# Kernel optimization log

Hardware: AMD Instinct MI355X
Metric: run time of the kernel (lower is better)

Reference implementation:

```python
import jax, jax.numpy as jnp
import numpy as np

# Propagation forward (reference path), with:
#   pairwise_fn       = dot product over feature dim: scores[b,i,j] = <val[b,i], val[b,j]>
#   edge_compress_fn  = softsign(x) = x / (1 + |x|)
#   val_proj/state_proj = Identity, return_delta = True
# Output: concat(delta_val [B,N,D], delta_state [B,N,1]) -> [B,N,D+1]

B, N, D = 4, 4096, 256


def setup_inputs() -> dict:
    key = jax.random.key(0)
    k1, k2 = jax.random.split(key)
    val = jax.random.normal(k1, (B, N, D), dtype=jnp.float32)
    state = jax.random.normal(k2, (B, N), dtype=jnp.float32)
    return {"val": val, "state": state}


def reference(val, state):
    # pairwise scores over all node pairs: [B, N, N]
    scores = jnp.einsum("bid,bjd->bij", val, val)
    # softsign edge compression
    edges = scores / (1.0 + jnp.abs(scores))
    # delta_state[b,i] = sum_j edges[b,i,j] * state[b,j]
    delta_state = jnp.einsum("bij,bj->bi", edges, state)
    # delta_val[b,i,d] = sum_j edges[b,i,j] * val[b,j,d]
    delta_val = jnp.einsum("bij,bjd->bid", edges, val)
    return jnp.concatenate([delta_val, delta_state[..., None]], axis=-1)
```

## Files before the change

kernel.cpp:

```cpp
#include <hip/hip_runtime.h>
#include <stdint.h>

#define BATCH 4
#define NN 4096
#define DD 256
#define TI 128
#define TJ 64
#define JS 2
#define JRANGE (NN / JS)
#define NITER (JRANGE / TJ)

#define VS_OFF 0
#define VT_OFF 65536
#define P_OFF  131072
#define LDS_BYTES 163840

typedef __attribute__((ext_vector_type(8))) short bf16x8;
typedef __attribute__((ext_vector_type(4))) float f32x4;
typedef __attribute__((ext_vector_type(4))) float f4v;
typedef __attribute__((ext_vector_type(8))) short s8v;
typedef __attribute__((ext_vector_type(4))) short s4v;

__device__ __forceinline__ short f2bf(float f) {
    uint32_t u = __builtin_bit_cast(uint32_t, f);
    u = (u + 0x7fffu + ((u >> 16) & 1u)) >> 16;
    return (short)u;
}

__device__ __forceinline__ void g2l16(const void* g, void* l) {
    __builtin_amdgcn_global_load_lds((const __attribute__((address_space(1))) void*)g,
                                     (__attribute__((address_space(3))) void*)l, 16, 0, 0);
}

__global__ __launch_bounds__(256) void prep_k(const float* __restrict__ val,
                                              short* __restrict__ vbf,
                                              short* __restrict__ vt) {
    __shared__ float tile[32][33];
    int b = blockIdx.z;
    int d0 = blockIdx.x * 32, n0 = blockIdx.y * 32;
    int tx = threadIdx.x, ty = threadIdx.y;
#pragma unroll
    for (int yy = ty; yy < 32; yy += 8) {
        float v = val[((size_t)b * NN + n0 + yy) * DD + d0 + tx];
        tile[yy][tx] = v;
        vbf[((size_t)b * NN + n0 + yy) * DD + d0 + tx] = f2bf(v);
    }
    __syncthreads();
#pragma unroll
    for (int yy = ty; yy < 32; yy += 8)
        vt[((size_t)b * DD + d0 + yy) * NN + n0 + tx] = f2bf(tile[tx][yy]);
}

__global__ void __launch_bounds__(512, 2) prop_main(const short* __restrict__ vbf,
                                                    const short* __restrict__ vtbf,
                                                    const float* __restrict__ state,
                                                    float* __restrict__ part,
                                                    float* __restrict__ spart) {
    extern __shared__ char smem[];

    const int raw = blockIdx.x;
    const int bid = ((raw & 7) << 5) | (raw >> 3);
    const int js = (bid >> 5) & 1;
    const int rb = bid & 31;
    const int b = bid >> 6;
    const int tid = threadIdx.x;
    const int w = tid >> 6, lane = tid & 63;
    const int g = lane >> 4, c = lane & 15;
    const int ig = w & 3, jh = w >> 2;
    const int wr = w & 1, wd = w >> 1;
    const int r7 = c & 7;
    const int j0base = js * JRANGE;

    const int xE = ((((r7 >> 2) << 2) | (g ^ (r7 & 3))) << 4);
    const int xO = (((((r7 >> 2) ^ 1) << 2) | (g ^ (r7 & 3))) << 4);

    bf16x8 Bf[2][8];
    const size_t irowb = (size_t)b * NN + rb * TI + ig * 32;
#pragma unroll
    for (int m = 0; m < 2; ++m)
#pragma unroll
        for (int k = 0; k < 8; ++k)
            Bf[m][k] = *(const bf16x8*)(vbf + ((irowb + m * 16 + c) * DD + k * 32 + g * 8));

    f32x4 accO[4][4];
#pragma unroll
    for (int mt = 0; mt < 4; ++mt)
#pragma unroll
        for (int dt = 0; dt < 4; ++dt)
            accO[mt][dt] = (f32x4){0.f, 0.f, 0.f, 0.f};
    float vsum[2] = {0.f, 0.f};

    auto stageVs = [&](int t, int nb) {
        const int j0 = j0base + t * TJ;
        char* dst = smem + VS_OFF + nb * 32768;
#pragma unroll
        for (int p = 0; p < 4; ++p) {
            int ch0 = p * 512 + w * 64;
            int ch = ch0 + lane;
            int row = ch >> 5, cir = ch & 31;
            g2l16(vbf + ((size_t)(b * NN + j0 + row) * DD + ((cir ^ (row & 7)) * 8)),
                  dst + ch0 * 16);
        }
    };
    auto stageVt = [&](int t, int nb) {
        const int j0 = j0base + t * TJ;
        char* dst = smem + VT_OFF + nb * 32768;
#pragma unroll
        for (int p = 0; p < 4; ++p) {
            int ch0 = p * 512 + w * 64;
            int ch = ch0 + lane;
            int d = ch >> 3, cj = ch & 7;
            g2l16(vtbf + ((size_t)(b * DD + d) * NN + j0 + ((cj ^ (d & 7)) * 8)),
                  dst + ch0 * 16);
        }
    };

    auto pvStep = [&](int slot) {
        const char* paRow = smem + P_OFF + slot * 16384 + (wr * 64 + c) * 128;
        const char* vbRow = smem + VT_OFF + slot * 32768 + (wd * 64 + c) * 128;
        __builtin_amdgcn_s_setprio(1);
#pragma unroll
        for (int kk = 0; kk < 2; ++kk) {
            const int off = kk ? xO : xE;
            bf16x8 pa[4], vb[4];
#pragma unroll
            for (int mt = 0; mt < 4; ++mt) pa[mt] = *(const bf16x8*)(paRow + mt * 2048 + off);
#pragma unroll
            for (int dt = 0; dt < 4; ++dt) vb[dt] = *(const bf16x8*)(vbRow + dt * 2048 + off);
#pragma unroll
            for (int mt = 0; mt < 4; ++mt)
#pragma unroll
                for (int dt = 0; dt < 4; ++dt)
                    accO[mt][dt] = __builtin_amdgcn_mfma_f32_16x16x32_bf16(pa[mt], vb[dt], accO[mt][dt], 0, 0, 0);
        }
        __builtin_amdgcn_s_setprio(0);
    };

    const float* stp = state + b * NN + j0base;

    stageVs(0, 0);
    stageVt(0, 0);
    __syncthreads();

    for (int t = 0; t < NITER; ++t) {
        const int cur = t & 1, prv = cur ^ 1;

        if (t + 1 < NITER) stageVs(t + 1, prv);

        f4v sv0 = *(const f4v*)(stp + t * TJ + jh * 32 + g * 4);
        f4v sv1 = *(const f4v*)(stp + t * TJ + jh * 32 + 16 + g * 4);

        if (t > 0) pvStep(prv);

        f32x4 accS[2][2];
#pragma unroll
        for (int jbl = 0; jbl < 2; ++jbl)
#pragma unroll
            for (int m = 0; m < 2; ++m)
                accS[jbl][m] = (f32x4){0.f, 0.f, 0.f, 0.f};

        const char* aRow0 = smem + VS_OFF + cur * 32768 + (jh * 32 + c) * 512;
        __builtin_amdgcn_s_setprio(1);
#pragma unroll
        for (int k = 0; k < 8; ++k) {
            const int off = (k >> 1) * 128 + ((k & 1) ? xO : xE);
            bf16x8 a0 = *(const bf16x8*)(aRow0 + off);
            bf16x8 a1 = *(const bf16x8*)(aRow0 + 8192 + off);
            accS[0][0] = __builtin_amdgcn_mfma_f32_16x16x32_bf16(a0, Bf[0][k], accS[0][0], 0, 0, 0);
            accS[0][1] = __builtin_amdgcn_mfma_f32_16x16x32_bf16(a0, Bf[1][k], accS[0][1], 0, 0, 0);
            accS[1][0] = __builtin_amdgcn_mfma_f32_16x16x32_bf16(a1, Bf[0][k], accS[1][0], 0, 0, 0);
            accS[1][1] = __builtin_amdgcn_mfma_f32_16x16x32_bf16(a1, Bf[1][k], accS[1][1], 0, 0, 0);
        }
        __builtin_amdgcn_s_setprio(0);

#pragma unroll
        for (int jbl = 0; jbl < 2; ++jbl) {
            f4v sv = jbl ? sv1 : sv0;
#pragma unroll
            for (int m = 0; m < 2; ++m) {
                s4v pk;
#pragma unroll
                for (int r = 0; r < 4; ++r) {
                    float s = accS[jbl][m][r];
                    float e = s * __builtin_amdgcn_rcpf(1.0f + __builtin_fabsf(s));
                    vsum[m] += e * sv[r];
                    pk[r] = f2bf(e);
                }
                int i = ig * 32 + m * 16 + c;
                *(s4v*)(smem + P_OFF + cur * 16384 + i * 128 +
                        ((jh * 64 + jbl * 32 + g * 8) ^ (r7 << 4))) = pk;
            }
        }

        __syncthreads();

        if (t + 1 < NITER) stageVt(t + 1, prv);
    }

    pvStep((NITER - 1) & 1);

    {
        float* po = part + (((size_t)(js * BATCH + b) * NN + rb * TI + wr * 64) * DD) + wd * 64;
#pragma unroll
        for (int mt = 0; mt < 4; ++mt)
#pragma unroll
            for (int dt = 0; dt < 4; ++dt)
#pragma unroll
                for (int r = 0; r < 4; ++r)
                    po[(size_t)(mt * 16 + g * 4 + r) * DD + dt * 16 + c] = accO[mt][dt][r];
    }

#pragma unroll
    for (int m = 0; m < 2; ++m) {
        vsum[m] += __shfl_xor(vsum[m], 16);
        vsum[m] += __shfl_xor(vsum[m], 32);
    }
    float* Xf = (float*)(smem + P_OFF);
    __syncthreads();
    if (jh == 1 && lane < 16) {
        Xf[(ig * 2 + 0) * 16 + lane] = vsum[0];
        Xf[(ig * 2 + 1) * 16 + lane] = vsum[1];
    }
    __syncthreads();
    if (jh == 0 && lane < 16) {
        size_t sb = ((size_t)js * BATCH + b) * NN + rb * TI + ig * 32;
#pragma unroll
        for (int m = 0; m < 2; ++m)
            spart[sb + m * 16 + lane] = vsum[m] + Xf[(ig * 2 + m) * 16 + lane];
    }
}

__global__ __launch_bounds__(256) void reduce2_k(const float* __restrict__ part,
                                                 const float* __restrict__ spart,
                                                 float* __restrict__ out) {
    const int row = blockIdx.x;
    const int t = threadIdx.x;
    const size_t PS = (size_t)BATCH * NN * DD;
    float v = part[(size_t)row * DD + t] + part[PS + (size_t)row * DD + t];
    out[(size_t)row * 257 + t] = v;
    if (t == 0) {
        const size_t SS = (size_t)BATCH * NN;
        out[(size_t)row * 257 + 256] = spart[row] + spart[SS + row];
    }
}

extern "C" void kernel_launch(void* const* d_in, const int* in_sizes, int n_in,
                              void* d_out, int out_size, void* d_ws, size_t ws_size,
                              hipStream_t stream) {
    const float* val = (const float*)d_in[0];
    const float* state = (const float*)d_in[1];
    float* out = (float*)d_out;

    const size_t bf_bytes = (size_t)BATCH * NN * DD * 2;
    const size_t part_bytes = (size_t)JS * BATCH * NN * DD * 4;
    const size_t spart_bytes = (size_t)JS * BATCH * NN * 4;
    short* vbf = (short*)d_ws;
    short* vtbf = (short*)((char*)d_ws + bf_bytes);
    float* part = (float*)((char*)d_ws + 2 * bf_bytes);
    float* spart = (float*)((char*)d_ws + 2 * bf_bytes + part_bytes);
    if (ws_size < 2 * bf_bytes + part_bytes + spart_bytes) return;

    hipFuncSetAttribute((const void*)prop_main, hipFuncAttributeMaxDynamicSharedMemorySize, LDS_BYTES);

    prep_k<<<dim3(DD / 32, NN / 32, BATCH), dim3(32, 8), 0, stream>>>(val, vbf, vtbf);
    prop_main<<<BATCH * (NN / TI) * JS, 512, LDS_BYTES, stream>>>(vbf, vtbf, state, part, spart);
    reduce2_k<<<BATCH * NN, 256, 0, stream>>>(part, spart, out);
}
```

Baseline: 94.41 us.

## Double workgroup to 1024 threads and repartition score/PV work across 16 waves

Prop kernel now runs 16 waves per block instead of 8. Each wave computes a 16x32 score tile and a 32x64 output tile, halving per-wave accumulators and staging loads. The score MFMAs are moved ahead of the previous PV step, and setprio is dropped around them. The state partial sums are reduced across four j-quarters through LDS. Launch bounds (1024,4) ask for fewer registers per thread, which may cause spills. LDS usage per block is unchanged, so resident waves per CU go up but blocks per CU may not.

```diff
diff --git a/kernel.cpp b/kernel.cpp
--- a/kernel.cpp
+++ b/kernel.cpp
@@ -31,6 +31,10 @@
     __builtin_amdgcn_global_load_lds((const __attribute__((address_space(1))) void*)g,
                                      (__attribute__((address_space(3))) void*)l, 16, 0, 0);
 }
+__device__ __forceinline__ void g2l4(const void* g, void* l) {
+    __builtin_amdgcn_global_load_lds((const __attribute__((address_space(1))) void*)g,
+                                     (__attribute__((address_space(3))) void*)l, 4, 0, 0);
+}
 
 __global__ __launch_bounds__(256) void prep_k(const float* __restrict__ val,
                                               short* __restrict__ vbf,
@@ -51,11 +55,11 @@
         vt[((size_t)b * DD + d0 + yy) * NN + n0 + tx] = f2bf(tile[tx][yy]);
 }
 
-__global__ void __launch_bounds__(512, 2) prop_main(const short* __restrict__ vbf,
-                                                    const short* __restrict__ vtbf,
-                                                    const float* __restrict__ state,
-                                                    float* __restrict__ part,
-                                                    float* __restrict__ spart) {
+__global__ void __launch_bounds__(1024, 4) prop_main(const short* __restrict__ vbf,
+                                                     const short* __restrict__ vtbf,
+                                                     const float* __restrict__ state,
+                                                     float* __restrict__ part,
+                                                     float* __restrict__ spart) {
     extern __shared__ char smem[];
 
     const int raw = blockIdx.x;
@@ -66,8 +70,8 @@
     const int tid = threadIdx.x;
     const int w = tid >> 6, lane = tid & 63;
     const int g = lane >> 4, c = lane & 15;
-    const int ig = w & 3, jh = w >> 2;
-    const int wr = w & 1, wd = w >> 1;
+    const int jq = w & 3, ip = w >> 2;
+    const int id = w >> 2, dq = w & 3;
     const int r7 = c & 7;
     const int j0base = js * JRANGE;
 
@@ -75,16 +79,16 @@
     const int xO = (((((r7 >> 2) ^ 1) << 2) | (g ^ (r7 & 3))) << 4);
 
     bf16x8 Bf[2][8];
-    const size_t irowb = (size_t)b * NN + rb * TI + ig * 32;
+    const size_t irowb = (size_t)b * NN + rb * TI + ip * 32;
 #pragma unroll
     for (int m = 0; m < 2; ++m)
 #pragma unroll
         for (int k = 0; k < 8; ++k)
             Bf[m][k] = *(const bf16x8*)(vbf + ((irowb + m * 16 + c) * DD + k * 32 + g * 8));
 
-    f32x4 accO[4][4];
-#pragma unroll
-    for (int mt = 0; mt < 4; ++mt)
+    f32x4 accO[2][4];
+#pragma unroll
+    for (int mt = 0; mt < 2; ++mt)
 #pragma unroll
         for (int dt = 0; dt < 4; ++dt)
             accO[mt][dt] = (f32x4){0.f, 0.f, 0.f, 0.f};
@@ -94,8 +98,8 @@
         const int j0 = j0base + t * TJ;
         char* dst = smem + VS_OFF + nb * 32768;
 #pragma unroll
-        for (int p = 0; p < 4; ++p) {
-            int ch0 = p * 512 + w * 64;
+        for (int p = 0; p < 2; ++p) {
+            int ch0 = p * 1024 + w * 64;
             int ch = ch0 + lane;
             int row = ch >> 5, cir = ch & 31;
             g2l16(vbf + ((size_t)(b * NN + j0 + row) * DD + ((cir ^ (row & 7)) * 8)),
@@ -106,8 +110,8 @@
         const int j0 = j0base + t * TJ;
         char* dst = smem + VT_OFF + nb * 32768;
 #pragma unroll
-        for (int p = 0; p < 4; ++p) {
-            int ch0 = p * 512 + w * 64;
+        for (int p = 0; p < 2; ++p) {
+            int ch0 = p * 1024 + w * 64;
             int ch = ch0 + lane;
             int d = ch >> 3, cj = ch & 7;
             g2l16(vtbf + ((size_t)(b * DD + d) * NN + j0 + ((cj ^ (d & 7)) * 8)),
@@ -116,19 +120,19 @@
     };
 
     auto pvStep = [&](int slot) {
-        const char* paRow = smem + P_OFF + slot * 16384 + (wr * 64 + c) * 128;
-        const char* vbRow = smem + VT_OFF + slot * 32768 + (wd * 64 + c) * 128;
+        const char* paRow = smem + P_OFF + slot * 16384 + (id * 32 + c) * 128;
+        const char* vbRow = smem + VT_OFF + slot * 32768 + (dq * 64 + c) * 128;
         __builtin_amdgcn_s_setprio(1);
 #pragma unroll
         for (int kk = 0; kk < 2; ++kk) {
             const int off = kk ? xO : xE;
-            bf16x8 pa[4], vb[4];
-#pragma unroll
-            for (int mt = 0; mt < 4; ++mt) pa[mt] = *(const bf16x8*)(paRow + mt * 2048 + off);
+            bf16x8 pa[2], vb[4];
+#pragma unroll
+            for (int mt = 0; mt < 2; ++mt) pa[mt] = *(const bf16x8*)(paRow + mt * 2048 + off);
 #pragma unroll
             for (int dt = 0; dt < 4; ++dt) vb[dt] = *(const bf16x8*)(vbRow + dt * 2048 + off);
 #pragma unroll
-            for (int mt = 0; mt < 4; ++mt)
+            for (int mt = 0; mt < 2; ++mt)
 #pragma unroll
                 for (int dt = 0; dt < 4; ++dt)
                     accO[mt][dt] = __builtin_amdgcn_mfma_f32_16x16x32_bf16(pa[mt], vb[dt], accO[mt][dt], 0, 0, 0);
@@ -147,49 +151,36 @@
 
         if (t + 1 < NITER) stageVs(t + 1, prv);
 
-        f4v sv0 = *(const f4v*)(stp + t * TJ + jh * 32 + g * 4);
-        f4v sv1 = *(const f4v*)(stp + t * TJ + jh * 32 + 16 + g * 4);
-
-        if (t > 0) pvStep(prv);
-
-        f32x4 accS[2][2];
-#pragma unroll
-        for (int jbl = 0; jbl < 2; ++jbl)
-#pragma unroll
-            for (int m = 0; m < 2; ++m)
-                accS[jbl][m] = (f32x4){0.f, 0.f, 0.f, 0.f};
-
-        const char* aRow0 = smem + VS_OFF + cur * 32768 + (jh * 32 + c) * 512;
-        __builtin_amdgcn_s_setprio(1);
+        f4v sv = *(const f4v*)(stp + t * TJ + jq * 16 + g * 4);
+
+        f32x4 accS[2];
+        accS[0] = (f32x4){0.f, 0.f, 0.f, 0.f};
+        accS[1] = (f32x4){0.f, 0.f, 0.f, 0.f};
+
+        const char* aRow0 = smem + VS_OFF + cur * 32768 + (jq * 16 + c) * 512;
 #pragma unroll
         for (int k = 0; k < 8; ++k) {
             const int off = (k >> 1) * 128 + ((k & 1) ? xO : xE);
             bf16x8 a0 = *(const bf16x8*)(aRow0 + off);
-            bf16x8 a1 = *(const bf16x8*)(aRow0 + 8192 + off);
-            accS[0][0] = __builtin_amdgcn_mfma_f32_16x16x32_bf16(a0, Bf[0][k], accS[0][0], 0, 0, 0);
-            accS[0][1] = __builtin_amdgcn_mfma_f32_16x16x32_bf16(a0, Bf[1][k], accS[0][1], 0, 0, 0);
-            accS[1][0] = __builtin_amdgcn_mfma_f32_16x16x32_bf16(a1, Bf[0][k], accS[1][0], 0, 0, 0);
-            accS[1][1] = __builtin_amdgcn_mfma_f32_16x16x32_bf16(a1, Bf[1][k], accS[1][1], 0, 0, 0);
-        }
-        __builtin_amdgcn_s_setprio(0);
-
-#pragma unroll
-        for (int jbl = 0; jbl < 2; ++jbl) {
-            f4v sv = jbl ? sv1 : sv0;
-#pragma unroll
-            for (int m = 0; m < 2; ++m) {
-                s4v pk;
-#pragma unroll
-                for (int r = 0; r < 4; ++r) {
-                    float s = accS[jbl][m][r];
-                    float e = s * __builtin_amdgcn_rcpf(1.0f + __builtin_fabsf(s));
-                    vsum[m] += e * sv[r];
-                    pk[r] = f2bf(e);
-                }
-                int i = ig * 32 + m * 16 + c;
-                *(s4v*)(smem + P_OFF + cur * 16384 + i * 128 +
-                        ((jh * 64 + jbl * 32 + g * 8) ^ (r7 << 4))) = pk;
+            accS[0] = __builtin_amdgcn_mfma_f32_16x16x32_bf16(a0, Bf[0][k], accS[0], 0, 0, 0);
+            accS[1] = __builtin_amdgcn_mfma_f32_16x16x32_bf16(a0, Bf[1][k], accS[1], 0, 0, 0);
+        }
+
+        if (t > 0) pvStep(prv);
+
+#pragma unroll
+        for (int m = 0; m < 2; ++m) {
+            s4v pk;
+#pragma unroll
+            for (int r = 0; r < 4; ++r) {
+                float s = accS[m][r];
+                float e = s * __builtin_amdgcn_rcpf(1.0f + __builtin_fabsf(s));
+                vsum[m] += e * sv[r];
+                pk[r] = f2bf(e);
             }
+            int i = ip * 32 + m * 16 + c;
+            *(s4v*)(smem + P_OFF + cur * 16384 + i * 128 +
+                    ((jq * 32 + g * 8) ^ (r7 << 4))) = pk;
         }
 
         __syncthreads();
@@ -200,9 +191,9 @@
     pvStep((NITER - 1) & 1);
 
     {
-        float* po = part + (((size_t)(js * BATCH + b) * NN + rb * TI + wr * 64) * DD) + wd * 64;
-#pragma unroll
-        for (int mt = 0; mt < 4; ++mt)
+        float* po = part + (((size_t)(js * BATCH + b) * NN + rb * TI + id * 32) * DD) + dq * 64;
+#pragma unroll
+        for (int mt = 0; mt < 2; ++mt)
 #pragma unroll
             for (int dt = 0; dt < 4; ++dt)
 #pragma unroll
@@ -217,16 +208,21 @@
     }
     float* Xf = (float*)(smem + P_OFF);
     __syncthreads();
-    if (jh == 1 && lane < 16) {
-        Xf[(ig * 2 + 0) * 16 + lane] = vsum[0];
-        Xf[(ig * 2 + 1) * 16 + lane] = vsum[1];
-    }
-    __syncthreads();
-    if (jh == 0 && lane < 16) {
-        size_t sb = ((size_t)js * BATCH + b) * NN + rb * TI + ig * 32;
-#pragma unroll
-        for (int m = 0; m < 2; ++m)
-            spart[sb + m * 16 + lane] = vsum[m] + Xf[(ig * 2 + m) * 16 + lane];
+    if (lane < 16) {
+        Xf[((jq * 4 + ip) * 2 + 0) * 16 + lane] = vsum[0];
+        Xf[((jq * 4 + ip) * 2 + 1) * 16 + lane] = vsum[1];
+    }
+    __syncthreads();
+    if (jq == 0 && lane < 16) {
+        size_t sb = ((size_t)js * BATCH + b) * NN + rb * TI + ip * 32;
+#pragma unroll
+        for (int m = 0; m < 2; ++m) {
+            float acc = 0.f;
+#pragma unroll
+            for (int q = 0; q < 4; ++q)
+                acc += Xf[((q * 4 + ip) * 2 + m) * 16 + lane];
+            spart[sb + m * 16 + lane] = acc;
+        }
     }
 }
 
@@ -263,6 +259,6 @@
     hipFuncSetAttribute((const void*)prop_main, hipFuncAttributeMaxDynamicSharedMemorySize, LDS_BYTES);
 
     prep_k<<<dim3(DD / 32, NN / 32, BATCH), dim3(32, 8), 0, stream>>>(val, vbf, vtbf);
-    prop_main<<<BATCH * (NN / TI) * JS, 512, LDS_BYTES, stream>>>(vbf, vtbf, state, part, spart);
+    prop_main<<<BATCH * (NN / TI) * JS, 1024, LDS_BYTES, stream>>>(vbf, vtbf, state, part, spart);
     reduce2_k<<<BATCH * NN, 256, 0, stream>>>(part, spart, out);
 }
```

Result: slower. 196.6 us (+108.3%).
